# Optimization experiments

Hardware: AMD Instinct MI355X
Metric: run time of the kernel (lower is better)

## Reference

```python
import jax, jax.numpy as jnp
import numpy as np

S, B, D, H, DH, E, F = 2048, 2, 512, 8, 64, 8, 1024
TOPK = 2


def setup_inputs() -> dict:
    key = jax.random.key(0)
    ks = jax.random.split(key, 12)
    rn = lambda k, shp, s=0.02: jax.random.normal(k, shp, jnp.float32) * s
    # RoPE tables (half-split convention): (S, DH)
    pos = jnp.arange(S, dtype=jnp.float32)[:, None]
    inv_freq = 1.0 / (10000.0 ** (jnp.arange(0, DH, 2, dtype=jnp.float32) / DH))
    ang = pos * inv_freq[None, :]                       # (S, DH//2)
    cos = jnp.concatenate([jnp.cos(ang), jnp.cos(ang)], axis=-1)
    sin = jnp.concatenate([jnp.sin(ang), jnp.sin(ang)], axis=-1)
    return {
        "src": jax.random.normal(ks[0], (S, B, D), jnp.float32),
        "cos": cos, "sin": sin,
        "Wq": rn(ks[1], (D, D)), "bq": jnp.zeros((D,), jnp.float32),
        "Wk": rn(ks[2], (D, D)), "bk": jnp.zeros((D,), jnp.float32),
        "Wv": rn(ks[3], (D, D)), "bv": jnp.zeros((D,), jnp.float32),
        "Wo": rn(ks[4], (D, D)), "bo": jnp.zeros((D,), jnp.float32),
        "ln1_g": jnp.ones((D,), jnp.float32), "ln1_b": jnp.zeros((D,), jnp.float32),
        "ln2_g": jnp.ones((D,), jnp.float32), "ln2_b": jnp.zeros((D,), jnp.float32),
        "Wg": rn(ks[5], (D, E)),
        "W1": rn(ks[6], (E, D, F)), "B1": jnp.zeros((E, F), jnp.float32),
        "W2": rn(ks[7], (E, F, D)), "B2": jnp.zeros((E, D), jnp.float32),
    }


def _layernorm(x, g, b, eps=1e-5):
    m = x.mean(-1, keepdims=True)
    v = ((x - m) ** 2).mean(-1, keepdims=True)
    return (x - m) * jax.lax.rsqrt(v + eps) * g + b


def _rotate_half(x):
    x1, x2 = jnp.split(x, 2, axis=-1)
    return jnp.concatenate([-x2, x1], axis=-1)


def _forward(src, cos, sin, Wq, bq, Wk, bk, Wv, bv, Wo, bo,
             ln1_g, ln1_b, ln2_g, ln2_b, Wg, W1, B1, W2, B2):
    # ---- RoPE self-attention ----
    q = (src @ Wq + bq).reshape(S, B, H, DH)
    k = (src @ Wk + bk).reshape(S, B, H, DH)
    v = (src @ Wv + bv).reshape(S, B, H, DH)
    c = cos[:, None, None, :]
    s = sin[:, None, None, :]
    q = q * c + _rotate_half(q) * s
    k = k * c + _rotate_half(k) * s
    scores = jnp.einsum("sbhd,tbhd->bhst", q, k) / jnp.sqrt(jnp.float32(DH))
    attn = jax.nn.softmax(scores, axis=-1)              # (B,H,S,S)
    ctx = jnp.einsum("bhst,tbhd->sbhd", attn, v).reshape(S, B, D)
    attn_out = ctx @ Wo + bo
    x = _layernorm(src + attn_out, ln1_g, ln1_b)
    # ---- MoE feed-forward (top-k softmax gating) ----
    xt = x.reshape(S * B, D)                            # (N, D)
    probs = jax.nn.softmax(xt @ Wg, axis=-1)            # (N, E)
    top_v, top_i = jax.lax.top_k(probs, TOPK)           # (N, TOPK)
    top_v = top_v / top_v.sum(-1, keepdims=True)
    N = S * B
    gates = jnp.zeros((N, E), jnp.float32).at[
        jnp.arange(N)[:, None], top_i].add(top_v)       # (N, E)
    h = jax.nn.relu(jnp.einsum("nd,edf->nef", xt, W1) + B1[None])   # (N,E,F)
    eo = jnp.einsum("nef,efd->ned", h, W2) + B2[None]               # (N,E,D)
    moe_out = jnp.einsum("ne,ned->nd", gates, eo).reshape(S, B, D)
    return _layernorm(x + moe_out, ln2_g, ln2_b)


def reference(src, cos, sin, Wq, bq, Wk, bk, Wv, bv, Wo, bo,
              ln1_g, ln1_b, ln2_g, ln2_b, Wg, W1, B1, W2, B2):
    return _forward(src, cos, sin, Wq, bq, Wk, bk, Wv, bv, Wo, bo,
                    ln1_g, ln1_b, ln2_g, ln2_b, Wg, W1, B1, W2, B2)
```

## Files before the change

kernel.cpp:

```cpp
#include <hip/hip_runtime.h>
#include <math.h>

#define S_  2048
#define B_  2
#define D_  512
#define H_  8
#define DH_ 64
#define E_  8
#define F_  1024
#define N_  4096
#define NPAIR_ 8192

typedef __attribute__((ext_vector_type(4))) float f32x4;
typedef __attribute__((ext_vector_type(8))) short short8;
typedef unsigned short u16;

__device__ __forceinline__ u16 f2bf(float f) {
  unsigned u = __builtin_bit_cast(unsigned, f);
  u += 0x7fffu + ((u >> 16) & 1u);
  return (u16)(u >> 16);
}
__device__ __forceinline__ float bf2f(u16 h) {
  unsigned u = ((unsigned)h) << 16;
  return __builtin_bit_cast(float, u);
}

__global__ __launch_bounds__(256) void src_split(const float* __restrict__ in,
                                                 u16* __restrict__ hi,
                                                 u16* __restrict__ lo) {
  size_t i = ((size_t)blockIdx.x * 256 + threadIdx.x) * 8;
  float f[8];
  *(float4*)&f[0] = *(const float4*)&in[i];
  *(float4*)&f[4] = *(const float4*)&in[i + 4];
  short8 h, l;
#pragma unroll
  for (int j = 0; j < 8; ++j) {
    u16 a = f2bf(f[j]);
    h[j] = (short)a;
    l[j] = (short)f2bf(f[j] - bf2f(a));
  }
  *(short8*)&hi[i] = h;
  *(short8*)&lo[i] = l;
}

__global__ __launch_bounds__(256) void wsplit_t(const float* __restrict__ W,
                                                u16* __restrict__ Whi,
                                                u16* __restrict__ Wlo,
                                                int Nn, int K) {
  __shared__ u16 Th[64][72];
  __shared__ u16 Tl[64][72];
  int kb = blockIdx.y * 64, nb = blockIdx.x * 64;
  int r = threadIdx.x >> 2, c0 = (threadIdx.x & 3) * 16;
  const float* wp = &W[(size_t)(kb + r) * Nn + nb + c0];
#pragma unroll
  for (int c = 0; c < 16; c += 4) {
    float4 t = *(const float4*)&wp[c];
    float f[4] = {t.x, t.y, t.z, t.w};
#pragma unroll
    for (int j = 0; j < 4; ++j) {
      u16 a = f2bf(f[j]);
      Th[r][c0 + c + j] = a;
      Tl[r][c0 + c + j] = f2bf(f[j] - bf2f(a));
    }
  }
  __syncthreads();
  short8 h0, h1, l0, l1;
#pragma unroll
  for (int j = 0; j < 8; ++j) {
    h0[j] = (short)Th[c0 + j][r];     h1[j] = (short)Th[c0 + 8 + j][r];
    l0[j] = (short)Tl[c0 + j][r];     l1[j] = (short)Tl[c0 + 8 + j][r];
  }
  size_t ob = (size_t)(nb + r) * K + kb + c0;
  *(short8*)&Whi[ob] = h0;  *(short8*)&Whi[ob + 8] = h1;
  *(short8*)&Wlo[ob] = l0;  *(short8*)&Wlo[ob + 8] = l1;
}

__global__ __launch_bounds__(256) void wtrans(const float* __restrict__ W,
                                              u16* __restrict__ Wt,
                                              int K, int Nn) {
  size_t eo = (size_t)blockIdx.z * K * Nn;
  __shared__ u16 T[64][72];
  int kb = blockIdx.y * 64, nb = blockIdx.x * 64;
  int r = threadIdx.x >> 2, c0 = (threadIdx.x & 3) * 16;
  const float* wp = &W[eo + (size_t)(kb + r) * Nn + nb + c0];
#pragma unroll
  for (int c = 0; c < 16; c += 4) {
    float4 t = *(const float4*)&wp[c];
    T[r][c0 + c + 0] = f2bf(t.x);
    T[r][c0 + c + 1] = f2bf(t.y);
    T[r][c0 + c + 2] = f2bf(t.z);
    T[r][c0 + c + 3] = f2bf(t.w);
  }
  __syncthreads();
  short8 s0, s1;
#pragma unroll
  for (int j = 0; j < 8; ++j) {
    s0[j] = (short)T[c0 + j][r];
    s1[j] = (short)T[c0 + 8 + j][r];
  }
  *(short8*)&Wt[eo + (size_t)(nb + r) * K + kb + c0] = s0;
  *(short8*)&Wt[eo + (size_t)(nb + r) * K + kb + c0 + 8] = s1;
}

__global__ __launch_bounds__(256) void qkv_mfma(const u16* __restrict__ Ah_g,
                                                const u16* __restrict__ Al_g,
                                                const u16* __restrict__ Bh_g,
                                                const u16* __restrict__ Bl_g,
                                                const float* __restrict__ bq,
                                                const float* __restrict__ bk,
                                                const float* __restrict__ bv,
                                                const float* __restrict__ cosb,
                                                const float* __restrict__ sinb,
                                                u16* __restrict__ qh, u16* __restrict__ ql,
                                                u16* __restrict__ kh, u16* __restrict__ kl,
                                                u16* __restrict__ vb) {
  __shared__ u16 Ah[128][40], Al[128][40], Bh[128][40], Bl[128][40];
  int tid = threadIdx.x;
  int w = tid >> 6, l = tid & 63;
  int wr = w >> 1, wc = w & 1;
  int lg = l >> 4, lx = l & 15;
  int m0 = blockIdx.x * 128, n0 = blockIdx.y * 128;
  int sr = tid >> 1, s16 = (tid & 1) * 16;
  const u16* Aph = Ah_g + (size_t)(m0 + sr) * 512;
  const u16* Apl = Al_g + (size_t)(m0 + sr) * 512;
  const u16* Bph = Bh_g + (size_t)(n0 + sr) * 512;
  const u16* Bpl = Bl_g + (size_t)(n0 + sr) * 512;
  f32x4 acc[4][4];
#pragma unroll
  for (int m = 0; m < 4; ++m)
#pragma unroll
    for (int n = 0; n < 4; ++n) acc[m][n] = (f32x4){0.f, 0.f, 0.f, 0.f};
  short8 ah0 = *(const short8*)&Aph[s16];
  short8 ah1 = *(const short8*)&Aph[s16 + 8];
  short8 al0 = *(const short8*)&Apl[s16];
  short8 al1 = *(const short8*)&Apl[s16 + 8];
  short8 bh0 = *(const short8*)&Bph[s16];
  short8 bh1 = *(const short8*)&Bph[s16 + 8];
  short8 bl0 = *(const short8*)&Bpl[s16];
  short8 bl1 = *(const short8*)&Bpl[s16 + 8];
  for (int k0 = 0; k0 < 512; k0 += 32) {
    __syncthreads();
    *(short8*)&Ah[sr][s16] = ah0; *(short8*)&Ah[sr][s16 + 8] = ah1;
    *(short8*)&Al[sr][s16] = al0; *(short8*)&Al[sr][s16 + 8] = al1;
    *(short8*)&Bh[sr][s16] = bh0; *(short8*)&Bh[sr][s16 + 8] = bh1;
    *(short8*)&Bl[sr][s16] = bl0; *(short8*)&Bl[sr][s16 + 8] = bl1;
    __syncthreads();
    if (k0 + 32 < 512) {
      int ko = k0 + 32 + s16;
      ah0 = *(const short8*)&Aph[ko]; ah1 = *(const short8*)&Aph[ko + 8];
      al0 = *(const short8*)&Apl[ko]; al1 = *(const short8*)&Apl[ko + 8];
      bh0 = *(const short8*)&Bph[ko]; bh1 = *(const short8*)&Bph[ko + 8];
      bl0 = *(const short8*)&Bpl[ko]; bl1 = *(const short8*)&Bpl[ko + 8];
    }
    short8 fah[4], fal[4], fbh[4], fbl[4];
#pragma unroll
    for (int m = 0; m < 4; ++m) {
      fah[m] = *(const short8*)&Ah[wr * 64 + m * 16 + lx][lg * 8];
      fal[m] = *(const short8*)&Al[wr * 64 + m * 16 + lx][lg * 8];
    }
#pragma unroll
    for (int n = 0; n < 4; ++n) {
      fbh[n] = *(const short8*)&Bh[wc * 64 + n * 16 + lx][lg * 8];
      fbl[n] = *(const short8*)&Bl[wc * 64 + n * 16 + lx][lg * 8];
    }
#pragma unroll
    for (int m = 0; m < 4; ++m)
#pragma unroll
      for (int n = 0; n < 4; ++n) {
        acc[m][n] = __builtin_amdgcn_mfma_f32_16x16x32_bf16(fah[m], fbh[n], acc[m][n], 0, 0, 0);
        acc[m][n] = __builtin_amdgcn_mfma_f32_16x16x32_bf16(fal[m], fbh[n], acc[m][n], 0, 0, 0);
        acc[m][n] = __builtin_amdgcn_mfma_f32_16x16x32_bf16(fah[m], fbl[n], acc[m][n], 0, 0, 0);
      }
  }
  int tcolbase = n0 + wc * 64;
  int tsel = tcolbase >> 9;
  int hbase = tcolbase & 511;
  const float* bias = (tsel == 0) ? bq : (tsel == 1) ? bk : bv;
  if (tsel == 2) {
#pragma unroll
    for (int m = 0; m < 4; ++m)
#pragma unroll
      for (int i = 0; i < 4; ++i) {
        int row = m0 + wr * 64 + m * 16 + lg * 4 + i;
#pragma unroll
        for (int n = 0; n < 4; ++n) {
          int col = hbase + n * 16 + lx;
          vb[(size_t)row * 512 + col] = f2bf(acc[m][n][i] + bias[col]);
        }
      }
  } else {
    u16* oh = tsel ? kh : qh;
    u16* ol = tsel ? kl : ql;
    float qsc = tsel ? 1.f : 0.125f;
#pragma unroll
    for (int m = 0; m < 4; ++m)
#pragma unroll
      for (int i = 0; i < 4; ++i) {
        int row = m0 + wr * 64 + m * 16 + lg * 4 + i;
        int s = row >> 1;
#pragma unroll
        for (int n = 0; n < 2; ++n) {
          int dln = n * 16 + lx;
          float c  = cosb[s * 64 + dln];
          float sn = sinb[s * 64 + dln];
          float a  = acc[m][n][i]     + bias[hbase + dln];
          float b2 = acc[m][n + 2][i] + bias[hbase + dln + 32];
          float ra = (a * c - b2 * sn) * qsc;
          float rb = (b2 * c + a * sn) * qsc;
          size_t ix = (size_t)row * 512 + hbase + dln;
          u16 rah = f2bf(ra);
          oh[ix] = rah; ol[ix] = f2bf(ra - bf2f(rah));
          u16 rbh = f2bf(rb);
          oh[ix + 32] = rbh; ol[ix + 32] = f2bf(rb - bf2f(rbh));
        }
      }
  }
}

__global__ __launch_bounds__(256) void attn_mfma2(const u16* __restrict__ qh,
                                                  const u16* __restrict__ ql,
                                                  const u16* __restrict__ kh,
                                                  const u16* __restrict__ kl,
                                                  const u16* __restrict__ vbuf,
                                                  u16* __restrict__ poh,
                                                  u16* __restrict__ pol,
                                                  float* __restrict__ pml) {
  __shared__ u16 Khi[64][72];
  __shared__ u16 Klo[64][72];
  __shared__ u16 Vt[64][72];
  __shared__ unsigned P2[4][16][32];
  int tid = threadIdx.x;
  int w = tid >> 6, l = tid & 63;
  int lg = l >> 4, lx = l & 15;
  int f = blockIdx.x;
  int xcd = f & 7, j = f >> 3;
  int slab = xcd + 8 * (j & 3);
  int qt = j >> 2;
  int bh = slab >> 1, kvh = slab & 1;
  int b = bh >> 3, h = bh & 7;

  short8 qfh[2], qfl[2];
  {
    int qrow = qt * 64 + w * 16 + lx;
    size_t qo = (size_t)(qrow * 2 + b) * 512 + h * 64 + lg * 8;
    qfh[0] = *(const short8*)&qh[qo];
    qfh[1] = *(const short8*)&qh[qo + 32];
    qfl[0] = *(const short8*)&ql[qo];
    qfl[1] = *(const short8*)&ql[qo + 32];
  }

  f32x4 o_acc[4];
#pragma unroll
  for (int dg = 0; dg < 4; ++dg) o_acc[dg] = (f32x4){0.f, 0.f, 0.f, 0.f};
  float m_run = -1e30f, l_run = 0.f;

  int kvr = tid >> 2, ds4 = (tid & 3) * 16;
  int kvc = tid & 63, dsg = (tid >> 6) * 16;
  int psw = (lx & 7) << 2;

  short8 rkh0, rkh1, rkl0, rkl1, rv0, rv1;
  {
    int t0 = kvh * 1024;
    size_t ko = (size_t)((t0 + kvr) * 2 + b) * 512 + h * 64 + ds4;
    rkh0 = *(const short8*)&kh[ko]; rkh1 = *(const short8*)&kh[ko + 8];
    rkl0 = *(const short8*)&kl[ko]; rkl1 = *(const short8*)&kl[ko + 8];
    size_t vo = (size_t)((t0 + kvc) * 2 + b) * 512 + h * 64 + dsg;
    rv0 = *(const short8*)&vbuf[vo]; rv1 = *(const short8*)&vbuf[vo + 8];
  }

  for (int tt = 0; tt < 1024; tt += 64) {
    __syncthreads();
    *(short8*)&Khi[kvr][ds4]     = rkh0;
    *(short8*)&Khi[kvr][ds4 + 8] = rkh1;
    *(short8*)&Klo[kvr][ds4]     = rkl0;
    *(short8*)&Klo[kvr][ds4 + 8] = rkl1;
#pragma unroll
    for (int c = 0; c < 8; ++c) {
      Vt[dsg + c][kvc] = (u16)rv0[c];
      Vt[dsg + 8 + c][kvc] = (u16)rv1[c];
    }
    __syncthreads();
    if (tt + 64 < 1024) {
      int t0 = kvh * 1024 + tt + 64;
      size_t ko = (size_t)((t0 + kvr) * 2 + b) * 512 + h * 64 + ds4;
      rkh0 = *(const short8*)&kh[ko]; rkh1 = *(const short8*)&kh[ko + 8];
      rkl0 = *(const short8*)&kl[ko]; rkl1 = *(const short8*)&kl[ko + 8];
      size_t vo = (size_t)((t0 + kvc) * 2 + b) * 512 + h * 64 + dsg;
      rv0 = *(const short8*)&vbuf[vo]; rv1 = *(const short8*)&vbuf[vo + 8];
    }

    f32x4 sc[4];
#pragma unroll
    for (int cg = 0; cg < 4; ++cg) {
      short8 kf0 = *(const short8*)&Khi[cg * 16 + lx][lg * 8];
      short8 kf1 = *(const short8*)&Khi[cg * 16 + lx][32 + lg * 8];
      short8 kg0 = *(const short8*)&Klo[cg * 16 + lx][lg * 8];
      short8 kg1 = *(const short8*)&Klo[cg * 16 + lx][32 + lg * 8];
      f32x4 a = (f32x4){0.f, 0.f, 0.f, 0.f};
      a = __builtin_amdgcn_mfma_f32_16x16x32_bf16(kf0, qfh[0], a, 0, 0, 0);
      a = __builtin_amdgcn_mfma_f32_16x16x32_bf16(kf1, qfh[1], a, 0, 0, 0);
      a = __builtin_amdgcn_mfma_f32_16x16x32_bf16(kf0, qfl[0], a, 0, 0, 0);
      a = __builtin_amdgcn_mfma_f32_16x16x32_bf16(kf1, qfl[1], a, 0, 0, 0);
      a = __builtin_amdgcn_mfma_f32_16x16x32_bf16(kg0, qfh[0], a, 0, 0, 0);
      a = __builtin_amdgcn_mfma_f32_16x16x32_bf16(kg1, qfh[1], a, 0, 0, 0);
      sc[cg] = a;
    }

    float tm = sc[0][0];
#pragma unroll
    for (int cg = 0; cg < 4; ++cg)
#pragma unroll
      for (int i = 0; i < 4; ++i) tm = fmaxf(tm, sc[cg][i]);
    tm = fmaxf(tm, __shfl_xor(tm, 16));
    tm = fmaxf(tm, __shfl_xor(tm, 32));
    float mn = fmaxf(m_run, tm);
    float corr = __expf(m_run - mn);
    m_run = mn;
    float ts = 0.f;
#pragma unroll
    for (int cg = 0; cg < 4; ++cg)
#pragma unroll
      for (int i = 0; i < 4; ++i) {
        float pv = __expf(sc[cg][i] - mn);
        sc[cg][i] = pv;
        ts += pv;
      }
    ts += __shfl_xor(ts, 16);
    ts += __shfl_xor(ts, 32);
    l_run = l_run * corr + ts;
#pragma unroll
    for (int dg = 0; dg < 4; ++dg) o_acc[dg] *= corr;

#pragma unroll
    for (int cg = 0; cg < 4; ++cg)
#pragma unroll
      for (int t = 0; t < 2; ++t) {
        unsigned dw = (unsigned)f2bf(sc[cg][2 * t]) |
                      ((unsigned)f2bf(sc[cg][2 * t + 1]) << 16);
        P2[w][lx][(8 * cg + 2 * lg + t) ^ psw] = dw;
      }
    short8 pf0 = *(const short8*)&P2[w][lx][(4 * lg) ^ psw];
    short8 pf1 = *(const short8*)&P2[w][lx][(16 + 4 * lg) ^ psw];

#pragma unroll
    for (int dg = 0; dg < 4; ++dg) {
      short8 v0 = *(const short8*)&Vt[dg * 16 + lx][lg * 8];
      short8 v1 = *(const short8*)&Vt[dg * 16 + lx][32 + lg * 8];
      o_acc[dg] = __builtin_amdgcn_mfma_f32_16x16x32_bf16(v0, pf0, o_acc[dg], 0, 0, 0);
      o_acc[dg] = __builtin_amdgcn_mfma_f32_16x16x32_bf16(v1, pf1, o_acc[dg], 0, 0, 0);
    }
  }

  {
    int qrow = qt * 64 + w * 16 + lx;
    int row2 = qrow * 2 + b;
    size_t base = (size_t)kvh * ((size_t)N_ * D_) + (size_t)row2 * 512 + h * 64;
#pragma unroll
    for (int dg = 0; dg < 4; ++dg)
#pragma unroll
      for (int i = 0; i < 4; ++i) {
        int d = dg * 16 + 4 * lg + i;
        float val = o_acc[dg][i];
        u16 hi = f2bf(val);
        poh[base + d] = hi;
        pol[base + d] = f2bf(val - bf2f(hi));
      }
    if (lg == 0) {
      int u = row2 * 8 + h;
      pml[(size_t)kvh * 65536 + u * 2 + 0] = m_run;
      pml[(size_t)kvh * 65536 + u * 2 + 1] = l_run;
    }
  }
}

__global__ __launch_bounds__(256) void merge_attn2(const u16* __restrict__ poh,
                                                   const u16* __restrict__ pol,
                                                   const float* __restrict__ pml,
                                                   u16* __restrict__ ch,
                                                   u16* __restrict__ cl) {
  int u = blockIdx.x * 4 + (threadIdx.x >> 6);
  int lane = threadIdx.x & 63;
  float m0 = pml[u * 2], l0 = pml[u * 2 + 1];
  float m1 = pml[65536 + u * 2], l1 = pml[65536 + u * 2 + 1];
  float m = fmaxf(m0, m1);
  float e0 = __expf(m0 - m), e1 = __expf(m1 - m);
  float inv = 1.f / (l0 * e0 + l1 * e1);
  int n = u >> 3, h = u & 7;
  size_t base = (size_t)n * 512 + h * 64 + lane;
  const size_t PO1 = (size_t)N_ * D_;
  float v0 = bf2f(poh[base]) + bf2f(pol[base]);
  float v1 = bf2f(poh[PO1 + base]) + bf2f(pol[PO1 + base]);
  float val = (v0 * e0 + v1 * e1) * inv;
  u16 hi = f2bf(val);
  ch[base] = hi;
  cl[base] = f2bf(val - bf2f(hi));
}

__global__ __launch_bounds__(256) void wo_mfma(const u16* __restrict__ Ah_g,
                                               const u16* __restrict__ Al_g,
                                               const u16* __restrict__ Bh_g,
                                               const u16* __restrict__ Bl_g,
                                               const float* __restrict__ bias,
                                               float* __restrict__ C) {
  __shared__ u16 Ah[128][40], Al[128][40], Bh[128][40], Bl[128][40];
  int tid = threadIdx.x;
  int w = tid >> 6, l = tid & 63;
  int wr = w >> 1, wc = w & 1;
  int lg = l >> 4, lx = l & 15;
  int m0 = blockIdx.x * 128, n0 = blockIdx.y * 128;
  int sr = tid >> 1, s16 = (tid & 1) * 16;
  const u16* Aph = Ah_g + (size_t)(m0 + sr) * 512;
  const u16* Apl = Al_g + (size_t)(m0 + sr) * 512;
  const u16* Bph = Bh_g + (size_t)(n0 + sr) * 512;
  const u16* Bpl = Bl_g + (size_t)(n0 + sr) * 512;
  f32x4 acc[4][4];
#pragma unroll
  for (int m = 0; m < 4; ++m)
#pragma unroll
    for (int n = 0; n < 4; ++n) acc[m][n] = (f32x4){0.f, 0.f, 0.f, 0.f};
  short8 ah0 = *(const short8*)&Aph[s16];
  short8 ah1 = *(const short8*)&Aph[s16 + 8];
  short8 al0 = *(const short8*)&Apl[s16];
  short8 al1 = *(const short8*)&Apl[s16 + 8];
  short8 bh0 = *(const short8*)&Bph[s16];
  short8 bh1 = *(const short8*)&Bph[s16 + 8];
  short8 bl0 = *(const short8*)&Bpl[s16];
  short8 bl1 = *(const short8*)&Bpl[s16 + 8];
  for (int k0 = 0; k0 < 512; k0 += 32) {
    __syncthreads();
    *(short8*)&Ah[sr][s16] = ah0; *(short8*)&Ah[sr][s16 + 8] = ah1;
    *(short8*)&Al[sr][s16] = al0; *(short8*)&Al[sr][s16 + 8] = al1;
    *(short8*)&Bh[sr][s16] = bh0; *(short8*)&Bh[sr][s16 + 8] = bh1;
    *(short8*)&Bl[sr][s16] = bl0; *(short8*)&Bl[sr][s16 + 8] = bl1;
    __syncthreads();
    if (k0 + 32 < 512) {
      int ko = k0 + 32 + s16;
      ah0 = *(const short8*)&Aph[ko]; ah1 = *(const short8*)&Aph[ko + 8];
      al0 = *(const short8*)&Apl[ko]; al1 = *(const short8*)&Apl[ko + 8];
      bh0 = *(const short8*)&Bph[ko]; bh1 = *(const short8*)&Bph[ko + 8];
      bl0 = *(const short8*)&Bpl[ko]; bl1 = *(const short8*)&Bpl[ko + 8];
    }
    short8 fah[4], fal[4], fbh[4], fbl[4];
#pragma unroll
    for (int m = 0; m < 4; ++m) {
      fah[m] = *(const short8*)&Ah[wr * 64 + m * 16 + lx][lg * 8];
      fal[m] = *(const short8*)&Al[wr * 64 + m * 16 + lx][lg * 8];
    }
#pragma unroll
    for (int n = 0; n < 4; ++n) {
      fbh[n] = *(const short8*)&Bh[wc * 64 + n * 16 + lx][lg * 8];
      fbl[n] = *(const short8*)&Bl[wc * 64 + n * 16 + lx][lg * 8];
    }
#pragma unroll
    for (int m = 0; m < 4; ++m)
#pragma unroll
      for (int n = 0; n < 4; ++n) {
        acc[m][n] = __builtin_amdgcn_mfma_f32_16x16x32_bf16(fah[m], fbh[n], acc[m][n], 0, 0, 0);
        acc[m][n] = __builtin_amdgcn_mfma_f32_16x16x32_bf16(fal[m], fbh[n], acc[m][n], 0, 0, 0);
        acc[m][n] = __builtin_amdgcn_mfma_f32_16x16x32_bf16(fah[m], fbl[n], acc[m][n], 0, 0, 0);
      }
  }
#pragma unroll
  for (int m = 0; m < 4; ++m)
#pragma unroll
    for (int i = 0; i < 4; ++i) {
      int row = m0 + wr * 64 + m * 16 + lg * 4 + i;
#pragma unroll
      for (int n = 0; n < 4; ++n) {
        int col = n0 + wc * 64 + n * 16 + lx;
        C[(size_t)row * 512 + col] = acc[m][n][i] + bias[col];
      }
    }
}

__global__ __launch_bounds__(256) void ln_res(const float* __restrict__ a,
                                              const float* __restrict__ b,
                                              const float* __restrict__ g,
                                              const float* __restrict__ beta,
                                              float* __restrict__ out,
                                              u16* __restrict__ obf) {
  int n = blockIdx.x * 4 + (threadIdx.x >> 6);
  int lane = threadIdx.x & 63;
  float v[8];
  float s = 0.f;
#pragma unroll
  for (int i = 0; i < 8; ++i) {
    int d = lane + 64 * i;
    v[i] = a[(size_t)n * D_ + d] + b[(size_t)n * D_ + d];
    s += v[i];
  }
#pragma unroll
  for (int m = 32; m; m >>= 1) s += __shfl_xor(s, m);
  float mean = s * (1.f / D_);
  float s2 = 0.f;
#pragma unroll
  for (int i = 0; i < 8; ++i) { float t = v[i] - mean; s2 += t * t; }
#pragma unroll
  for (int m = 32; m; m >>= 1) s2 += __shfl_xor(s2, m);
  float r = rsqrtf(s2 * (1.f / D_) + 1e-5f);
#pragma unroll
  for (int i = 0; i < 8; ++i) {
    int d = lane + 64 * i;
    float val = (v[i] - mean) * r * g[d] + beta[d];
    out[(size_t)n * D_ + d] = val;
    obf[(size_t)n * D_ + d] = f2bf(val);
  }
}

__global__ __launch_bounds__(256) void ln2_final(const float* __restrict__ x,
                                                 const u16* __restrict__ mp,
                                                 const float* __restrict__ g,
                                                 const float* __restrict__ beta,
                                                 float* __restrict__ out) {
  int n = blockIdx.x * 4 + (threadIdx.x >> 6);
  int lane = threadIdx.x & 63;
  float v[8];
  float s = 0.f;
#pragma unroll
  for (int i = 0; i < 8; ++i) {
    int d = lane + 64 * i;
    v[i] = x[(size_t)n * D_ + d] + bf2f(mp[(size_t)(2 * n) * D_ + d]) +
           bf2f(mp[(size_t)(2 * n + 1) * D_ + d]);
    s += v[i];
  }
#pragma unroll
  for (int m = 32; m; m >>= 1) s += __shfl_xor(s, m);
  float mean = s * (1.f / D_);
  float s2 = 0.f;
#pragma unroll
  for (int i = 0; i < 8; ++i) { float t = v[i] - mean; s2 += t * t; }
#pragma unroll
  for (int m = 32; m; m >>= 1) s2 += __shfl_xor(s2, m);
  float r = rsqrtf(s2 * (1.f / D_) + 1e-5f);
#pragma unroll
  for (int i = 0; i < 8; ++i) {
    int d = lane + 64 * i;
    out[(size_t)n * D_ + d] = (v[i] - mean) * r * g[d] + beta[d];
  }
}

__global__ __launch_bounds__(256) void gate_compute(const float* __restrict__ x,
                                                    const float* __restrict__ Wg,
                                                    float* __restrict__ gp,
                                                    int* __restrict__ tope) {
  int n = blockIdx.x * 4 + (threadIdx.x >> 6);
  int lane = threadIdx.x & 63;
  float p[E_] = {};
  for (int d = lane; d < D_; d += 64) {
    float xv = x[(size_t)n * D_ + d];
    const float* wr = &Wg[(size_t)d * E_];
#pragma unroll
    for (int e = 0; e < E_; ++e) p[e] += xv * wr[e];
  }
#pragma unroll
  for (int e = 0; e < E_; ++e)
#pragma unroll
    for (int m = 32; m; m >>= 1) p[e] += __shfl_xor(p[e], m);
  if (lane == 0) {
    float mx = p[0];
#pragma unroll
    for (int e = 1; e < E_; ++e) mx = fmaxf(mx, p[e]);
    float q[E_];
#pragma unroll
    for (int e = 0; e < E_; ++e) q[e] = expf(p[e] - mx);
    int e1 = 0;
#pragma unroll
    for (int e = 1; e < E_; ++e) if (q[e] > q[e1]) e1 = e;
    int e2 = (e1 == 0) ? 1 : 0;
#pragma unroll
    for (int e = 0; e < E_; ++e) if (e != e1 && q[e] > q[e2]) e2 = e;
    float denom = q[e1] + q[e2];
    gp[n * 2] = q[e1] / denom;
    gp[n * 2 + 1] = q[e2] / denom;
    tope[n] = e1 | (e2 << 8);
  }
}

__global__ __launch_bounds__(256) void route_build(const int* __restrict__ tope,
                                                   int* __restrict__ cnt,
                                                   int* __restrict__ lst) {
  int e = blockIdx.x;
  __shared__ int wsum[4];
  __shared__ int basem;
  int tid = threadIdx.x;
  int w = tid >> 6, lane = tid & 63;
  if (tid == 0) basem = 0;
  __syncthreads();
  for (int c0 = 0; c0 < N_; c0 += 256) {
    int n = c0 + tid;
    int te = tope[n];
    int e1 = te & 0xff, e2 = (te >> 8) & 0xff;
    bool m2 = (e2 == e);
    bool flag = (e1 == e) || m2;
    unsigned long long mask = __ballot(flag);
    int wpre = __popcll(mask & ((1ull << lane) - 1ull));
    if (lane == 0) wsum[w] = __popcll(mask);
    __syncthreads();
    int woff = 0;
    for (int i = 0; i < w; ++i) woff += wsum[i];
    int total = wsum[0] + wsum[1] + wsum[2] + wsum[3];
    if (flag) lst[e * N_ + basem + woff + wpre] = n * 2 + (m2 ? 1 : 0);
    __syncthreads();
    if (tid == 0) basem += total;
    __syncthreads();
  }
  if (tid == 0) cnt[e] = basem;
}

template <int MODE>
__global__ __launch_bounds__(256) void moe_mfma(const u16* __restrict__ Abase,
                                                const u16* __restrict__ Wt,
                                                const float* __restrict__ bias,
                                                const float* __restrict__ gp,
                                                u16* __restrict__ outp,
                                                const int* __restrict__ cnt,
                                                const int* __restrict__ lst) {
  constexpr int K  = MODE ? 1024 : 512;
  constexpr int Nn = MODE ? 512 : 1024;
  constexpr int NT = Nn / 128;
  constexpr int NI = K / 32;
  int fidx = blockIdx.x;
  int e = fidx & 7;
  int r = fidx >> 3;
  int nt = r % NT;
  int mt = r / NT;
  int c = cnt[e];
  int m0 = mt * 64;
  if (m0 >= c) return;
  int off = 0;
#pragma unroll
  for (int i = 0; i < E_; ++i) if (i < e) off += cnt[i];
  int n0 = nt * 128;
  __shared__ u16 As[64][40];
  __shared__ u16 Bs[128][40];
  int tid = threadIdx.x;
  int w = tid >> 6, l = tid & 63;
  int lg = l >> 4, lx = l & 15;
  int arow = tid >> 2, aseg = (tid & 3) * 8;
  int brow = tid >> 1, bseg = (tid & 1) * 16;
  int ar = m0 + arow; if (ar >= c) ar = c - 1;
  const u16* Ap;
  if (MODE == 0) Ap = Abase + (size_t)(lst[e * N_ + ar] >> 1) * 512 + aseg;
  else           Ap = Abase + (size_t)(off + ar) * 1024 + aseg;
  const u16* Bp = Wt + (size_t)e * K * Nn + (size_t)(n0 + brow) * K + bseg;

  f32x4 acc[4][2];
#pragma unroll
  for (int m = 0; m < 4; ++m)
#pragma unroll
    for (int n = 0; n < 2; ++n) acc[m][n] = (f32x4){0.f, 0.f, 0.f, 0.f};

  short8 pa  = *(const short8*)&Ap[0];
  short8 pb0 = *(const short8*)&Bp[0];
  short8 pb1 = *(const short8*)&Bp[8];
  for (int kk = 0; kk < NI; ++kk) {
    __syncthreads();
    *(short8*)&As[arow][aseg] = pa;
    *(short8*)&Bs[brow][bseg] = pb0;
    *(short8*)&Bs[brow][bseg + 8] = pb1;
    __syncthreads();
    if (kk + 1 < NI) {
      int ko = (kk + 1) * 32;
      pa  = *(const short8*)&Ap[ko];
      pb0 = *(const short8*)&Bp[ko];
      pb1 = *(const short8*)&Bp[ko + 8];
    }
    short8 af[4], bf[2];
#pragma unroll
    for (int m = 0; m < 4; ++m)
      af[m] = *(const short8*)&As[m * 16 + lx][lg * 8];
#pragma unroll
    for (int n = 0; n < 2; ++n)
      bf[n] = *(const short8*)&Bs[w * 32 + n * 16 + lx][lg * 8];
#pragma unroll
    for (int m = 0; m < 4; ++m)
#pragma unroll
      for (int n = 0; n < 2; ++n)
        acc[m][n] = __builtin_amdgcn_mfma_f32_16x16x32_bf16(af[m], bf[n], acc[m][n], 0, 0, 0);
  }
#pragma unroll
  for (int m = 0; m < 4; ++m)
#pragma unroll
    for (int i = 0; i < 4; ++i) {
      int rr = m0 + m * 16 + lg * 4 + i;
      if (rr < c) {
#pragma unroll
        for (int n = 0; n < 2; ++n) {
          int col = n0 + w * 32 + n * 16 + lx;
          float val = acc[m][n][i] + bias[e * Nn + col];
          if (MODE == 0) {
            outp[(size_t)(off + rr) * 1024 + col] = f2bf(fmaxf(val, 0.f));
          } else {
            int p = lst[e * N_ + rr];
            outp[(size_t)p * 512 + col] = f2bf(gp[p] * val);
          }
        }
      }
    }
}

extern "C" void kernel_launch(void* const* d_in, const int* in_sizes, int n_in,
                              void* d_out, int out_size, void* d_ws, size_t ws_size,
                              hipStream_t stream) {
  const float* src  = (const float*)d_in[0];
  const float* cosb = (const float*)d_in[1];
  const float* sinb = (const float*)d_in[2];
  const float* Wq   = (const float*)d_in[3];
  const float* bq   = (const float*)d_in[4];
  const float* Wk   = (const float*)d_in[5];
  const float* bk   = (const float*)d_in[6];
  const float* Wv   = (const float*)d_in[7];
  const float* bv   = (const float*)d_in[8];
  const float* Wo   = (const float*)d_in[9];
  const float* bo   = (const float*)d_in[10];
  const float* ln1g = (const float*)d_in[11];
  const float* ln1b = (const float*)d_in[12];
  const float* ln2g = (const float*)d_in[13];
  const float* ln2b = (const float*)d_in[14];
  const float* Wg   = (const float*)d_in[15];
  const float* W1   = (const float*)d_in[16];
  const float* B1   = (const float*)d_in[17];
  const float* W2   = (const float*)d_in[18];
  const float* B2   = (const float*)d_in[19];
  float* out = (float*)d_out;
  char* wsb = (char*)d_ws;

  const size_t MB1 = 1u << 20;
  u16* sh   = (u16*)(wsb + 0 * MB1);
  u16* sl   = (u16*)(wsb + 4 * MB1);
  u16* qhb  = (u16*)(wsb + 8 * MB1);
  u16* qlb  = (u16*)(wsb + 12 * MB1);
  u16* khb  = (u16*)(wsb + 16 * MB1);
  u16* klb  = (u16*)(wsb + 20 * MB1);
  u16* vbuf = (u16*)(wsb + 24 * MB1);
  u16* poh  = (u16*)(wsb + 28 * MB1);
  u16* pol  = (u16*)(wsb + 36 * MB1);
  float* pml = (float*)(wsb + 44 * MB1);
  float* aob = (float*)(wsb + 28 * MB1);
  float* xb  = (float*)(wsb + 36 * MB1);
  u16* xbf   = (u16*)(wsb + 44 * MB1);
  u16* Wqkv_hi = (u16*)(wsb + 48 * MB1);
  u16* Wqkv_lo = (u16*)(wsb + 48 * MB1 + 1572864);
  u16* Wo_hi   = (u16*)(wsb + 48 * MB1 + 3145728);
  u16* Wo_lo   = (u16*)(wsb + 48 * MB1 + 3670016);
  u16* W1t     = (u16*)(wsb + 52 * MB1);
  u16* W2t     = (u16*)(wsb + 28 * MB1);
  float* gpb   = (float*)(wsb + 60 * MB1);
  int* cnt     = (int*)(wsb + 60 * MB1 + 32768);
  int* lst     = (int*)(wsb + 60 * MB1 + 32768 + 64);
  int* tope    = (int*)(wsb + 60 * MB1 + 32768 + 64 + 131072);
  u16* ch  = sh;
  u16* cl  = sl;
  u16* hbf = (u16*)(wsb + 8 * MB1);
  u16* mp  = (u16*)(wsb + 0 * MB1);

  dim3 blk(256);
  src_split<<<dim3(1024), blk, 0, stream>>>(src, sh, sl);
  wsplit_t<<<dim3(8, 8), blk, 0, stream>>>(Wq, Wqkv_hi, Wqkv_lo, 512, 512);
  wsplit_t<<<dim3(8, 8), blk, 0, stream>>>(Wk, Wqkv_hi + 512 * 512, Wqkv_lo + 512 * 512, 512, 512);
  wsplit_t<<<dim3(8, 8), blk, 0, stream>>>(Wv, Wqkv_hi + 1024 * 512, Wqkv_lo + 1024 * 512, 512, 512);
  wsplit_t<<<dim3(8, 8), blk, 0, stream>>>(Wo, Wo_hi, Wo_lo, 512, 512);
  qkv_mfma<<<dim3(32, 12), blk, 0, stream>>>(sh, sl, Wqkv_hi, Wqkv_lo, bq, bk, bv,
                                             cosb, sinb, qhb, qlb, khb, klb, vbuf);
  attn_mfma2<<<dim3(1024), blk, 0, stream>>>(qhb, qlb, khb, klb, vbuf, poh, pol, pml);
  merge_attn2<<<dim3(8192), blk, 0, stream>>>(poh, pol, pml, ch, cl);
  wo_mfma<<<dim3(32, 4), blk, 0, stream>>>(ch, cl, Wo_hi, Wo_lo, bo, aob);
  ln_res<<<dim3(1024), blk, 0, stream>>>(src, aob, ln1g, ln1b, xb, xbf);
  wtrans<<<dim3(8, 16, 8), blk, 0, stream>>>(W2, W2t, 1024, 512);
  wtrans<<<dim3(16, 8, 8), blk, 0, stream>>>(W1, W1t, 512, 1024);
  gate_compute<<<dim3(1024), blk, 0, stream>>>(xb, Wg, gpb, tope);
  route_build<<<dim3(8), blk, 0, stream>>>(tope, cnt, lst);
  moe_mfma<0><<<dim3(8 * 8 * 64), blk, 0, stream>>>(xbf, W1t, B1, gpb, hbf, cnt, lst);
  moe_mfma<1><<<dim3(8 * 4 * 64), blk, 0, stream>>>(hbf, W2t, B2, gpb, mp, cnt, lst);
  ln2_final<<<dim3(1024), blk, 0, stream>>>(xb, mp, ln2g, ln2b, out);
}
```

Measured before the change: 237.8 us.

## Double attention query tile per block and fuse gating into LayerNorm

The attention kernel now runs 512 threads (8 waves) per block, each block covering 128 query rows instead of 64. The grid is halved, so each K/V tile staged in shared memory serves twice as many queries and global K/V traffic drops. Separately, the top-2 gating computation moves into the first residual LayerNorm kernel, which removes one launch and one re-read of the normalized activations. The larger blocks may lower occupancy and parallelism, since 512 blocks now span the GPU.

```diff
diff --git a/kernel.cpp b/kernel.cpp
--- a/kernel.cpp
+++ b/kernel.cpp
@@ -217,7 +217,7 @@
   }
 }
 
-__global__ __launch_bounds__(256) void attn_mfma2(const u16* __restrict__ qh,
+__global__ __launch_bounds__(512) void attn_mfma2(const u16* __restrict__ qh,
                                                   const u16* __restrict__ ql,
                                                   const u16* __restrict__ kh,
                                                   const u16* __restrict__ kl,
@@ -228,7 +228,7 @@
   __shared__ u16 Khi[64][72];
   __shared__ u16 Klo[64][72];
   __shared__ u16 Vt[64][72];
-  __shared__ unsigned P2[4][16][32];
+  __shared__ unsigned P2[8][16][32];
   int tid = threadIdx.x;
   int w = tid >> 6, l = tid & 63;
   int lg = l >> 4, lx = l & 15;
@@ -241,7 +241,7 @@
 
   short8 qfh[2], qfl[2];
   {
-    int qrow = qt * 64 + w * 16 + lx;
+    int qrow = qt * 128 + w * 16 + lx;
     size_t qo = (size_t)(qrow * 2 + b) * 512 + h * 64 + lg * 8;
     qfh[0] = *(const short8*)&qh[qo];
     qfh[1] = *(const short8*)&qh[qo + 32];
@@ -254,39 +254,34 @@
   for (int dg = 0; dg < 4; ++dg) o_acc[dg] = (f32x4){0.f, 0.f, 0.f, 0.f};
   float m_run = -1e30f, l_run = 0.f;
 
-  int kvr = tid >> 2, ds4 = (tid & 3) * 16;
-  int kvc = tid & 63, dsg = (tid >> 6) * 16;
+  int kvr = tid >> 3, ds4 = (tid & 7) * 8;
+  int kvc = tid & 63, dsg = (tid >> 6) * 8;
   int psw = (lx & 7) << 2;
 
-  short8 rkh0, rkh1, rkl0, rkl1, rv0, rv1;
+  short8 rkh, rkl, rv;
   {
     int t0 = kvh * 1024;
     size_t ko = (size_t)((t0 + kvr) * 2 + b) * 512 + h * 64 + ds4;
-    rkh0 = *(const short8*)&kh[ko]; rkh1 = *(const short8*)&kh[ko + 8];
-    rkl0 = *(const short8*)&kl[ko]; rkl1 = *(const short8*)&kl[ko + 8];
+    rkh = *(const short8*)&kh[ko];
+    rkl = *(const short8*)&kl[ko];
     size_t vo = (size_t)((t0 + kvc) * 2 + b) * 512 + h * 64 + dsg;
-    rv0 = *(const short8*)&vbuf[vo]; rv1 = *(const short8*)&vbuf[vo + 8];
+    rv = *(const short8*)&vbuf[vo];
   }
 
   for (int tt = 0; tt < 1024; tt += 64) {
     __syncthreads();
-    *(short8*)&Khi[kvr][ds4]     = rkh0;
-    *(short8*)&Khi[kvr][ds4 + 8] = rkh1;
-    *(short8*)&Klo[kvr][ds4]     = rkl0;
-    *(short8*)&Klo[kvr][ds4 + 8] = rkl1;
-#pragma unroll
-    for (int c = 0; c < 8; ++c) {
-      Vt[dsg + c][kvc] = (u16)rv0[c];
-      Vt[dsg + 8 + c][kvc] = (u16)rv1[c];
-    }
+    *(short8*)&Khi[kvr][ds4] = rkh;
+    *(short8*)&Klo[kvr][ds4] = rkl;
+#pragma unroll
+    for (int c = 0; c < 8; ++c) Vt[dsg + c][kvc] = (u16)rv[c];
     __syncthreads();
     if (tt + 64 < 1024) {
       int t0 = kvh * 1024 + tt + 64;
       size_t ko = (size_t)((t0 + kvr) * 2 + b) * 512 + h * 64 + ds4;
-      rkh0 = *(const short8*)&kh[ko]; rkh1 = *(const short8*)&kh[ko + 8];
-      rkl0 = *(const short8*)&kl[ko]; rkl1 = *(const short8*)&kl[ko + 8];
+      rkh = *(const short8*)&kh[ko];
+      rkl = *(const short8*)&kl[ko];
       size_t vo = (size_t)((t0 + kvc) * 2 + b) * 512 + h * 64 + dsg;
-      rv0 = *(const short8*)&vbuf[vo]; rv1 = *(const short8*)&vbuf[vo + 8];
+      rv = *(const short8*)&vbuf[vo];
     }
 
     f32x4 sc[4];
@@ -352,7 +347,7 @@
   }
 
   {
-    int qrow = qt * 64 + w * 16 + lx;
+    int qrow = qt * 128 + w * 16 + lx;
     int row2 = qrow * 2 + b;
     size_t base = (size_t)kvh * ((size_t)N_ * D_) + (size_t)row2 * 512 + h * 64;
 #pragma unroll
@@ -473,12 +468,15 @@
     }
 }
 
-__global__ __launch_bounds__(256) void ln_res(const float* __restrict__ a,
-                                              const float* __restrict__ b,
-                                              const float* __restrict__ g,
-                                              const float* __restrict__ beta,
-                                              float* __restrict__ out,
-                                              u16* __restrict__ obf) {
+__global__ __launch_bounds__(256) void ln_res_gate(const float* __restrict__ a,
+                                                   const float* __restrict__ b,
+                                                   const float* __restrict__ g,
+                                                   const float* __restrict__ beta,
+                                                   const float* __restrict__ Wg,
+                                                   float* __restrict__ out,
+                                                   u16* __restrict__ obf,
+                                                   float* __restrict__ gp,
+                                                   int* __restrict__ tope) {
   int n = blockIdx.x * 4 + (threadIdx.x >> 6);
   int lane = threadIdx.x & 63;
   float v[8];
@@ -498,12 +496,38 @@
 #pragma unroll
   for (int m = 32; m; m >>= 1) s2 += __shfl_xor(s2, m);
   float r = rsqrtf(s2 * (1.f / D_) + 1e-5f);
+  float p[E_] = {};
 #pragma unroll
   for (int i = 0; i < 8; ++i) {
     int d = lane + 64 * i;
     float val = (v[i] - mean) * r * g[d] + beta[d];
     out[(size_t)n * D_ + d] = val;
     obf[(size_t)n * D_ + d] = f2bf(val);
+    const float* wr = &Wg[(size_t)d * E_];
+#pragma unroll
+    for (int e = 0; e < E_; ++e) p[e] += val * wr[e];
+  }
+#pragma unroll
+  for (int e = 0; e < E_; ++e)
+#pragma unroll
+    for (int m = 32; m; m >>= 1) p[e] += __shfl_xor(p[e], m);
+  if (lane == 0) {
+    float mx = p[0];
+#pragma unroll
+    for (int e = 1; e < E_; ++e) mx = fmaxf(mx, p[e]);
+    float q[E_];
+#pragma unroll
+    for (int e = 0; e < E_; ++e) q[e] = expf(p[e] - mx);
+    int e1 = 0;
+#pragma unroll
+    for (int e = 1; e < E_; ++e) if (q[e] > q[e1]) e1 = e;
+    int e2 = (e1 == 0) ? 1 : 0;
+#pragma unroll
+    for (int e = 0; e < E_; ++e) if (e != e1 && q[e] > q[e2]) e2 = e;
+    float denom = q[e1] + q[e2];
+    gp[n * 2] = q[e1] / denom;
+    gp[n * 2 + 1] = q[e2] / denom;
+    tope[n] = e1 | (e2 << 8);
   }
 }
 
@@ -536,43 +560,6 @@
   for (int i = 0; i < 8; ++i) {
     int d = lane + 64 * i;
     out[(size_t)n * D_ + d] = (v[i] - mean) * r * g[d] + beta[d];
-  }
-}
-
-__global__ __launch_bounds__(256) void gate_compute(const float* __restrict__ x,
-                                                    const float* __restrict__ Wg,
-                                                    float* __restrict__ gp,
-                                                    int* __restrict__ tope) {
-  int n = blockIdx.x * 4 + (threadIdx.x >> 6);
-  int lane = threadIdx.x & 63;
-  float p[E_] = {};
-  for (int d = lane; d < D_; d += 64) {
-    float xv = x[(size_t)n * D_ + d];
-    const float* wr = &Wg[(size_t)d * E_];
-#pragma unroll
-    for (int e = 0; e < E_; ++e) p[e] += xv * wr[e];
-  }
-#pragma unroll
-  for (int e = 0; e < E_; ++e)
-#pragma unroll
-    for (int m = 32; m; m >>= 1) p[e] += __shfl_xor(p[e], m);
-  if (lane == 0) {
-    float mx = p[0];
-#pragma unroll
-    for (int e = 1; e < E_; ++e) mx = fmaxf(mx, p[e]);
-    float q[E_];
-#pragma unroll
-    for (int e = 0; e < E_; ++e) q[e] = expf(p[e] - mx);
-    int e1 = 0;
-#pragma unroll
-    for (int e = 1; e < E_; ++e) if (q[e] > q[e1]) e1 = e;
-    int e2 = (e1 == 0) ? 1 : 0;
-#pragma unroll
-    for (int e = 0; e < E_; ++e) if (e != e1 && q[e] > q[e2]) e2 = e;
-    float denom = q[e1] + q[e2];
-    gp[n * 2] = q[e1] / denom;
-    gp[n * 2 + 1] = q[e2] / denom;
-    tope[n] = e1 | (e2 << 8);
   }
 }
 
@@ -762,13 +749,12 @@
   wsplit_t<<<dim3(8, 8), blk, 0, stream>>>(Wo, Wo_hi, Wo_lo, 512, 512);
   qkv_mfma<<<dim3(32, 12), blk, 0, stream>>>(sh, sl, Wqkv_hi, Wqkv_lo, bq, bk, bv,
                                              cosb, sinb, qhb, qlb, khb, klb, vbuf);
-  attn_mfma2<<<dim3(1024), blk, 0, stream>>>(qhb, qlb, khb, klb, vbuf, poh, pol, pml);
+  attn_mfma2<<<dim3(512), dim3(512), 0, stream>>>(qhb, qlb, khb, klb, vbuf, poh, pol, pml);
   merge_attn2<<<dim3(8192), blk, 0, stream>>>(poh, pol, pml, ch, cl);
   wo_mfma<<<dim3(32, 4), blk, 0, stream>>>(ch, cl, Wo_hi, Wo_lo, bo, aob);
-  ln_res<<<dim3(1024), blk, 0, stream>>>(src, aob, ln1g, ln1b, xb, xbf);
+  ln_res_gate<<<dim3(1024), blk, 0, stream>>>(src, aob, ln1g, ln1b, Wg, xb, xbf, gpb, tope);
   wtrans<<<dim3(8, 16, 8), blk, 0, stream>>>(W2, W2t, 1024, 512);
   wtrans<<<dim3(16, 8, 8), blk, 0, stream>>>(W1, W1t, 512, 1024);
-  gate_compute<<<dim3(1024), blk, 0, stream>>>(xb, Wg, gpb, tope);
   route_build<<<dim3(8), blk, 0, stream>>>(tope, cnt, lst);
   moe_mfma<0><<<dim3(8 * 8 * 64), blk, 0, stream>>>(xbf, W1t, B1, gpb, hbf, cnt, lst);
   moe_mfma<1><<<dim3(8 * 4 * 64), blk, 0, stream>>>(hbf, W2t, B2, gpb, mp, cnt, lst);
```

Measured after the change: 227.2 us. 1.05x faster.
